# Kernel optimization log

Measured on AMD Instinct MI355X. Metric: run time of the kernel, lower is better.

Reference implementation:

```python
import jax, jax.numpy as jnp
import numpy as np

B, L, H = 256, 128, 512  # batch, max_len, hidden (en_hidden_size == de_hidden_size)


def setup_inputs() -> dict:
    key = jax.random.key(0)
    ks = jax.random.split(key, 12)
    xs = jax.random.randint(ks[0], (B, L), 0, 1000, dtype=jnp.int32)
    argsort_xs = jnp.argsort(xs, axis=1).astype(jnp.int32)  # teacher-forcing pointer targets
    x_lens = jnp.full((B,), L, dtype=jnp.int32)  # passed through but unused by the math
    s = 0.05
    p = lambda k, shp: jax.random.normal(k, shp, jnp.float32) * s
    return {
        "xs": xs, "x_lens": x_lens, "argsort_xs": argsort_xs,
        # encoder LSTM(1 -> H), PyTorch gate order i,f,g,o; b = b_ih + b_hh fused
        "enc_Wi": p(ks[1], (4 * H, 1)), "enc_Wh": p(ks[2], (4 * H, H)), "enc_b": p(ks[3], (4 * H,)),
        # decoder LSTM(H+1 -> H)
        "dec_Wi": p(ks[4], (4 * H, H + 1)), "dec_Wh": p(ks[5], (4 * H, H)), "dec_b": p(ks[6], (4 * H,)),
        # PtrNetAttention: w1, w2 [H,H] (bias-free Linear stores [out,in]), vt [1,H]
        "w1": p(ks[7], (H, H)), "w2": p(ks[8], (H, H)), "vt": p(ks[9], (1, H)),
    }


def _lstm_step(x, h, c, Wi, Wh, b):
    z = x @ Wi.T + h @ Wh.T + b
    i, f, g, o = jnp.split(z, 4, axis=-1)
    c = jax.nn.sigmoid(f) * c + jax.nn.sigmoid(i) * jnp.tanh(g)
    h = jax.nn.sigmoid(o) * jnp.tanh(c)
    return h, c


def _forward(xs, argsort_xs, enc_Wi, enc_Wh, enc_b, dec_Wi, dec_Wh, dec_b, w1, w2, vt):
    xf = xs.astype(jnp.float32)
    h0 = jnp.zeros((B, H), jnp.float32)
    c0 = jnp.zeros((B, H), jnp.float32)

    def enc_step(carry, x_t):
        h, c = carry
        h, c = _lstm_step(x_t[:, None], h, c, enc_Wi, enc_Wh, enc_b)
        return (h, c), h

    (h, c), enc_out = jax.lax.scan(enc_step, (h0, c0), xf.T)  # enc_out: [L,B,H]
    enc_out = enc_out.transpose(1, 0, 2)  # [B,L,H]
    enc_w1 = enc_out @ w1.T  # hoisted: w1(encoder_output), identical math each step

    def dec_step(carry, tf_idx):
        h, c, dec_in = carry
        # attention uses pre-update decoder hidden h (decoder_hidden[0][0])
        scores = jnp.tanh(enc_w1 + (h @ w2.T)[:, None, :]) @ vt[0]  # [B,L]
        aj = jax.nn.softmax(scores, axis=1)
        context = jnp.einsum('bl,blh->bh', aj, enc_out)
        x_in = jnp.concatenate([context, dec_in[:, None]], axis=-1)  # [B,H+1]
        h, c = _lstm_step(x_in, h, c, dec_Wi, dec_Wh, dec_b)
        # teacher-forced pointer: next input is xs[t, argsort_xs[t, i]]
        next_in = jnp.take_along_axis(xf, tf_idx[:, None], axis=1)[:, 0]
        return (h, c, next_in), jax.nn.log_softmax(scores, axis=1)

    dec_in0 = jnp.zeros((B,), jnp.float32)
    _, outs = jax.lax.scan(dec_step, (h, c, dec_in0), argsort_xs.T)  # [L,B,L]
    return outs.transpose(1, 0, 2)  # [B,L,L], matching decoder_outputs.permute(1,0,2)


def reference(xs, x_lens, argsort_xs, enc_Wi, enc_Wh, enc_b, dec_Wi, dec_Wh, dec_b, w1, w2, vt):
    return _forward(xs, argsort_xs, enc_Wi, enc_Wh, enc_b, dec_Wi, dec_Wh, dec_b, w1, w2, vt)
```

## Files before the change

### kernel.cpp

```cpp
#include <hip/hip_runtime.h>

#define BB 256
#define LL 128
#define HH 512
#define H4 2048

typedef unsigned short us;
typedef unsigned long long u64;
typedef __attribute__((ext_vector_type(8))) __bf16 bf16x8;
typedef __attribute__((ext_vector_type(4))) float f32x4;
typedef __attribute__((ext_vector_type(4))) int i32x4;

__device__ __forceinline__ float bf2f(us s) {
    unsigned u = ((unsigned)s) << 16;
    return __builtin_bit_cast(float, u);
}
__device__ __forceinline__ us f2bf(float f) {
    unsigned u = __builtin_bit_cast(unsigned, f);
    return (us)((u + 0x7fffu + ((u >> 16) & 1u)) >> 16);
}
__device__ __forceinline__ float sigm(float x) { return 1.f / (1.f + __expf(-x)); }
__device__ __forceinline__ float tanh_(float x) { return 1.f - 2.f / (1.f + __expf(2.f * x)); }
__device__ __forceinline__ bf16x8 ldb8(const us* p) { return *(const bf16x8*)(const void*)p; }

__device__ __forceinline__ bf16x8 ldb8_dev(const us* p) {
    union { u64 q[2]; bf16x8 v; } u;
    u.q[0] = __hip_atomic_load((const u64*)(const void*)p, __ATOMIC_RELAXED, __HIP_MEMORY_SCOPE_AGENT);
    u.q[1] = __hip_atomic_load((const u64*)(const void*)p + 1, __ATOMIC_RELAXED, __HIP_MEMORY_SCOPE_AGENT);
    return u.v;
}
__device__ __forceinline__ void st_pair_dev(us* p, unsigned myv, int lane) {
    unsigned ov = __shfl_xor(myv, 1);
    if (!(lane & 1)) {
        unsigned pk = (myv & 0xffffu) | (ov << 16);
        __hip_atomic_store((unsigned*)(void*)p, pk, __ATOMIC_RELAXED, __HIP_MEMORY_SCOPE_AGENT);
    }
}

__device__ __forceinline__ void gsync_nf(unsigned* flags, int myidx, int base, int n, unsigned target) {
    __syncthreads();
    if (threadIdx.x < 64) {
        if (threadIdx.x == 0)
            __hip_atomic_store(flags + (size_t)myidx * 16, target, __ATOMIC_RELAXED,
                               __HIP_MEMORY_SCOPE_AGENT);
        for (int i = (int)threadIdx.x; i < n; i += 64)
            while (__hip_atomic_load(flags + (size_t)(base + i) * 16, __ATOMIC_RELAXED,
                                     __HIP_MEMORY_SCOPE_AGENT) < target) {}
        asm volatile("" ::: "memory");
    }
    __syncthreads();
}

__device__ __forceinline__ void gsync_f(unsigned* flags, int myidx, int base, int n, unsigned target) {
    __syncthreads();
    if (threadIdx.x < 64) {
        if (threadIdx.x == 0) {
            __builtin_amdgcn_fence(__ATOMIC_RELEASE, "agent");
            __hip_atomic_store(flags + (size_t)myidx * 16, target, __ATOMIC_RELAXED,
                               __HIP_MEMORY_SCOPE_AGENT);
        }
        for (int i = (int)threadIdx.x; i < n; i += 64)
            while (__hip_atomic_load(flags + (size_t)(base + i) * 16, __ATOMIC_RELAXED,
                                     __HIP_MEMORY_SCOPE_AGENT) < target) {}
        __builtin_amdgcn_fence(__ATOMIC_ACQUIRE, "agent");
    }
    __syncthreads();
}

__device__ __forceinline__ bf16x8 ldfragA(const char* bufA, int l15, int quad, int kk) {
    int off = ((kk << 6) + (quad << 4)) ^ ((l15 & 7) << 4);
    return *(const bf16x8*)(bufA + (l15 << 10) + off);
}

extern "C" __global__ void __launch_bounds__(512) k_mega(
    const int* __restrict__ xs, const int* __restrict__ argsort,
    const float* __restrict__ enc_Wi, const float* __restrict__ enc_Wh, const float* __restrict__ enc_b,
    const float* __restrict__ dec_Wi, const float* __restrict__ dec_Wh, const float* __restrict__ dec_b,
    const float* __restrict__ w1, const float* __restrict__ w2, const float* __restrict__ vt,
    float* __restrict__ out, char* __restrict__ ws) {
    unsigned* flags = (unsigned*)ws;
    float* din = (float*)(ws + 524288);
    us* hdec = (us*)(ws + 526336);
    us* q = (us*)(ws + 1050624);
    us* ctx = (us*)(ws + 1312768);
    us* wiR = (us*)(ws + 1574912);
    float* wi_last = (float*)(ws + 3672064);
    us* whE = (us*)(ws + 3680256);
    us* whD = (us*)(ws + 5777408);
    us* w1B = (us*)(ws + 7874560);
    us* w2B = (us*)(ws + 8398848);
    us* enc_out = (us*)(ws + 8923136);
    us* enc_w1 = (us*)(ws + 42477568);

    extern __shared__ char smem[];
    us* eos = (us*)smem;
    char* bufA = smem + 131072;
    float* bufB = (float*)(smem + 147456);
    __shared__ float scs[LL];
    __shared__ float aj[LL];
    __shared__ float redm[2];
    __shared__ float reds[2];

    const int tid = threadIdx.x;
    const int lane = tid & 63;
    const int w = tid >> 6;
    const int l15 = lane & 15, quad = lane >> 4;
    const int blk = blockIdx.x;
    const int g = blk & 15;
    const int m = blk >> 4;
    const int b0 = g << 4;
    const int myflag = g * 16 + m;
    const int ct = w & 1;
    const int gate = w >> 1;
    const int c0 = ((m << 1) | ct) << 4;
    unsigned tgt = 0;

    auto stage_contig = [&](const us* src) {
        for (int e = tid; e < 1024; e += 512) {
            int row = e >> 6, bo = (e & 63) << 4;
            bf16x8 v = ldb8_dev(src + (e << 3));
            *(bf16x8*)(bufA + (row << 10) + (bo ^ ((row & 7) << 4))) = v;
        }
    };

    {
        int gt = blk * 512 + tid;
        for (int i = gt; i < H4 * HH; i += 131072) whE[i] = f2bf(enc_Wh[i]);
        for (int i = gt; i < H4 * HH; i += 131072) whD[i] = f2bf(dec_Wh[i]);
        for (int i = gt; i < HH * HH; i += 131072) w1B[i] = f2bf(w1[i]);
        for (int i = gt; i < HH * HH; i += 131072) w2B[i] = f2bf(w2[i]);
        for (int i = gt; i < H4 * HH; i += 131072)
            wiR[i] = f2bf(dec_Wi[(size_t)(i >> 9) * 513 + (i & 511)]);
        if (gt < H4) wi_last[gt] = dec_Wi[(size_t)gt * 513 + 512];
    }
    gsync_f(flags, myflag, 0, 256, ++tgt);

    float creg[4] = {0.f, 0.f, 0.f, 0.f};

    {
        bf16x8 whEf[16];
        {
            const us* Be = whE + (size_t)(gate * HH + c0 + l15) * HH + quad * 8;
#pragma unroll
            for (int kk = 0; kk < 16; ++kk) whEf[kk] = ldb8(Be + kk * 32);
        }
        float biE[4], wiE[4];
        if (w < 2) {
#pragma unroll
            for (int gg = 0; gg < 4; ++gg) {
                int rg = gg * HH + c0 + l15;
                biE[gg] = enc_b[rg];
                wiE[gg] = enc_Wi[rg];
            }
        }
        for (int t = 0; t < LL; ++t) {
            if (t > 0) {
                for (int e = tid; e < 1024; e += 512) {
                    int row = e >> 6, bo = (e & 63) << 4;
                    bf16x8 v = ldb8_dev(enc_out + ((size_t)(b0 + row) * LL + (t - 1)) * HH + (bo >> 1));
                    *(bf16x8*)(bufA + (row << 10) + (bo ^ ((row & 7) << 4))) = v;
                }
                __syncthreads();
                f32x4 acc = {};
#pragma unroll
                for (int kk = 0; kk < 16; ++kk)
                    acc = __builtin_amdgcn_mfma_f32_16x16x32_bf16(ldfragA(bufA, l15, quad, kk),
                                                                  whEf[kk], acc, 0, 0, 0);
#pragma unroll
                for (int r = 0; r < 4; ++r)
                    bufB[(ct * 4 + gate) * 256 + (quad * 4 + r) * 16 + l15] = acc[r];
                __syncthreads();
            }
            if (w < 2) {
#pragma unroll
                for (int r = 0; r < 4; ++r) {
                    int b = b0 + quad * 4 + r;
                    float xv = (float)xs[b * LL + t];
                    float zz[4];
#pragma unroll
                    for (int gg = 0; gg < 4; ++gg)
                        zz[gg] = (t > 0 ? bufB[(w * 4 + gg) * 256 + (quad * 4 + r) * 16 + l15] : 0.f)
                                 + biE[gg] + xv * wiE[gg];
                    float c_ = sigm(zz[1]) * creg[r] + sigm(zz[0]) * tanh_(zz[2]);
                    creg[r] = c_;
                    unsigned hv = (unsigned)f2bf(sigm(zz[3]) * tanh_(c_));
                    st_pair_dev(&enc_out[((size_t)b * LL + t) * HH + c0 + l15], hv, lane);
                    if (t == LL - 1) st_pair_dev(&hdec[(size_t)b * HH + c0 + l15], hv, lane);
                }
            }
            gsync_nf(flags, myflag, g * 16, 16, ++tgt);
        }
    }

    {
        int lw = m * 8 + w;
        for (int it = 0; it < 8; ++it) {
            int task = it * 128 + lw;
            int mt = task >> 3;
            int n0 = (task & 7) << 6;
            size_t m0 = (size_t)b0 * LL + (size_t)mt * 16;
            f32x4 acc[4] = {};
            const us* Ar = enc_out + (m0 + l15) * HH + quad * 8;
            const us* Br = w1B + (size_t)(n0 + l15) * HH + quad * 8;
#pragma unroll 8
            for (int kk = 0; kk < 16; ++kk) {
                bf16x8 a = ldb8(Ar + kk * 32);
#pragma unroll
                for (int tt = 0; tt < 4; ++tt) {
                    bf16x8 bv = ldb8(Br + (size_t)tt * 16 * HH + kk * 32);
                    acc[tt] = __builtin_amdgcn_mfma_f32_16x16x32_bf16(a, bv, acc[tt], 0, 0, 0);
                }
            }
#pragma unroll
            for (int tt = 0; tt < 4; ++tt)
#pragma unroll
                for (int r = 0; r < 4; ++r)
                    enc_w1[(m0 + quad * 4 + r) * HH + n0 + tt * 16 + l15] = f2bf(acc[tt][r]);
        }
    }
    gsync_f(flags, myflag, g * 16, 16, ++tgt);

    {
        const i32x4* src = (const i32x4*)(const void*)(enc_out + (size_t)(b0 + m) * LL * HH);
        i32x4* dst = (i32x4*)(void*)eos;
        for (int i = tid; i < 8192; i += 512) dst[i] = src[i];
    }
    bf16x8 ew1f[16];
    {
        const us* p = enc_w1 + ((size_t)(b0 + m) * LL + w) * HH + lane * 8;
#pragma unroll
        for (int i = 0; i < 16; ++i) ew1f[i] = ldb8(p + (size_t)i * 8 * HH);
    }
    __syncthreads();

    bf16x8 wiRf[16], whDf[16], w2f[4];
    {
        const us* Bw = wiR + (size_t)(gate * HH + c0 + l15) * HH + quad * 8;
        const us* Bh = whD + (size_t)(gate * HH + c0 + l15) * HH + quad * 8;
#pragma unroll
        for (int kk = 0; kk < 16; ++kk) {
            wiRf[kk] = ldb8(Bw + kk * 32);
            whDf[kk] = ldb8(Bh + kk * 32);
        }
        const us* Bq = w2B + (size_t)(c0 + l15) * HH + quad * 8;
#pragma unroll
        for (int j = 0; j < 4; ++j) w2f[j] = ldb8(Bq + (gate * 4 + j) * 32);
    }
    float biD[4], wlD[4];
    if (w < 2) {
#pragma unroll
        for (int gg = 0; gg < 4; ++gg) {
            int rg = gg * HH + c0 + l15;
            biD[gg] = dec_b[rg];
            wlD[gg] = wi_last[rg];
        }
    }

    for (int t = 0; t < LL; ++t) {
        const us* hcur = hdec + (size_t)(t & 1) * BB * HH;

        stage_contig(hcur + (size_t)b0 * HH);
        __syncthreads();
        {
            f32x4 acc = {};
#pragma unroll
            for (int j = 0; j < 4; ++j)
                acc = __builtin_amdgcn_mfma_f32_16x16x32_bf16(
                    ldfragA(bufA, l15, quad, gate * 4 + j), w2f[j], acc, 0, 0, 0);
#pragma unroll
            for (int r = 0; r < 4; ++r)
                bufB[(gate * 2 + ct) * 256 + (quad * 4 + r) * 16 + l15] = acc[r];
        }
        __syncthreads();
        if (w < 2) {
#pragma unroll
            for (int r = 0; r < 4; ++r) {
                float s = 0.f;
#pragma unroll
                for (int kq = 0; kq < 4; ++kq)
                    s += bufB[(kq * 2 + w) * 256 + (quad * 4 + r) * 16 + l15];
                st_pair_dev(&q[(size_t)(b0 + quad * 4 + r) * HH + c0 + l15],
                            (unsigned)f2bf(s), lane);
            }
        }
        gsync_nf(flags, myflag, g * 16, 16, ++tgt);

        {
            int b = b0 + m;
            int k0 = lane * 8;
            bf16x8 qv = ldb8_dev(q + (size_t)b * HH + k0);
            float qk[8], vtk[8];
#pragma unroll
            for (int j = 0; j < 8; ++j) {
                qk[j] = (float)qv[j];
                vtk[j] = vt[k0 + j];
            }
#pragma unroll 4
            for (int i = 0; i < 16; ++i) {
                int l = i * 8 + w;
                bf16x8 e8 = ew1f[i];
                float s = 0.f;
#pragma unroll
                for (int j = 0; j < 8; ++j) s += tanh_((float)e8[j] + qk[j]) * vtk[j];
#pragma unroll
                for (int off = 1; off < 64; off <<= 1) s += __shfl_xor(s, off);
                if (lane == 0) scs[l] = s;
            }
            __syncthreads();
            bool act = tid < 128;
            float sc = act ? scs[tid] : -1e30f;
            float mx = sc;
#pragma unroll
            for (int off = 1; off < 64; off <<= 1) mx = fmaxf(mx, __shfl_xor(mx, off));
            if (act && lane == 0) redm[w] = mx;
            __syncthreads();
            float M = fmaxf(redm[0], redm[1]);
            float e = act ? __expf(sc - M) : 0.f;
            float ss = e;
#pragma unroll
            for (int off = 1; off < 64; off <<= 1) ss += __shfl_xor(ss, off);
            if (act && lane == 0) reds[w] = ss;
            __syncthreads();
            float S = reds[0] + reds[1];
            if (act) {
                __builtin_nontemporal_store(sc - M - __logf(S), &out[((size_t)b * LL + t) * LL + tid]);
                aj[tid] = e / S;
            }
            __syncthreads();
            const us* ep = eos + tid;
            float cacc = 0.f;
#pragma unroll 16
            for (int l2 = 0; l2 < LL; ++l2) cacc += aj[l2] * bf2f(ep[(size_t)l2 * HH]);
            st_pair_dev(&ctx[(size_t)b * HH + tid], (unsigned)f2bf(cacc), tid & 63);
            if (tid == 0) {
                int idx = argsort[b * LL + t];
                __hip_atomic_store(&din[(size_t)((t + 1) & 1) * BB + b], (float)xs[b * LL + idx],
                                   __ATOMIC_RELAXED, __HIP_MEMORY_SCOPE_AGENT);
            }
        }
        gsync_nf(flags, myflag, g * 16, 16, ++tgt);

        {
            f32x4 zacc = {};
#pragma unroll
            for (int kk = 0; kk < 16; ++kk)
                zacc = __builtin_amdgcn_mfma_f32_16x16x32_bf16(ldfragA(bufA, l15, quad, kk),
                                                               whDf[kk], zacc, 0, 0, 0);
            __syncthreads();
            stage_contig(ctx + (size_t)b0 * HH);
            __syncthreads();
#pragma unroll
            for (int kk = 0; kk < 16; ++kk)
                zacc = __builtin_amdgcn_mfma_f32_16x16x32_bf16(ldfragA(bufA, l15, quad, kk),
                                                               wiRf[kk], zacc, 0, 0, 0);
#pragma unroll
            for (int r = 0; r < 4; ++r)
                bufB[(ct * 4 + gate) * 256 + (quad * 4 + r) * 16 + l15] = zacc[r];
        }
        __syncthreads();
        if (w < 2) {
            us* hnxt = hdec + (size_t)((t + 1) & 1) * BB * HH;
            const float* dcur = din + (size_t)(t & 1) * BB;
#pragma unroll
            for (int r = 0; r < 4; ++r) {
                int b = b0 + quad * 4 + r;
                float dv = (t == 0) ? 0.f
                                    : __hip_atomic_load((const float*)&dcur[b], __ATOMIC_RELAXED,
                                                        __HIP_MEMORY_SCOPE_AGENT);
                float zz[4];
#pragma unroll
                for (int gg = 0; gg < 4; ++gg)
                    zz[gg] = bufB[(w * 4 + gg) * 256 + (quad * 4 + r) * 16 + l15]
                             + biD[gg] + dv * wlD[gg];
                float c_ = sigm(zz[1]) * creg[r] + sigm(zz[0]) * tanh_(zz[2]);
                creg[r] = c_;
                st_pair_dev(&hnxt[(size_t)b * HH + c0 + l15],
                            (unsigned)f2bf(sigm(zz[3]) * tanh_(c_)), lane);
            }
        }
        gsync_nf(flags, myflag, g * 16, 16, ++tgt);
    }
}

extern "C" void kernel_launch(void* const* d_in, const int* in_sizes, int n_in,
                              void* d_out, int out_size, void* d_ws, size_t ws_size,
                              hipStream_t stream) {
    const int* xs = (const int*)d_in[0];
    const int* argsort = (const int*)d_in[2];
    const float* enc_Wi = (const float*)d_in[3];
    const float* enc_Wh = (const float*)d_in[4];
    const float* enc_b = (const float*)d_in[5];
    const float* dec_Wi = (const float*)d_in[6];
    const float* dec_Wh = (const float*)d_in[7];
    const float* dec_b = (const float*)d_in[8];
    const float* w1 = (const float*)d_in[9];
    const float* w2 = (const float*)d_in[10];
    const float* vt = (const float*)d_in[11];
    float* out = (float*)d_out;
    char* ws = (char*)d_ws;

    static bool attr_done = false;
    if (!attr_done) {
        hipFuncSetAttribute((const void*)k_mega, hipFuncAttributeMaxDynamicSharedMemorySize, 155648);
        attr_done = true;
    }

    hipMemsetAsync(ws, 0, 16384, stream);

    void* kargs[] = {&xs, &argsort, &enc_Wi, &enc_Wh, &enc_b, &dec_Wi, &dec_Wh, &dec_b,
                     &w1, &w2, &vt, &out, &ws};
    hipLaunchCooperativeKernel((void*)k_mega, dim3(256), dim3(512), kargs, 155648, stream);

    (void)in_sizes; (void)n_in; (void)out_size; (void)ws_size;
}
```

Baseline: 4.849 ms.

## Pack barrier flags contiguously, drop LDS enc_out staging, prefetch ctx into separate buffer

The grid-barrier flags are packed into contiguous words per group instead of one per 64-byte slot. Polling now uses 16 lanes with s_sleep backoff, which should cut cache-line traffic during the many per-step barriers. The 128KB LDS copy of enc_out is removed and the context reduction reads from global memory instead, so dynamic shared memory is no longer needed. Context rows are loaded into registers before the Wh MFMA and written to a second LDS buffer, which removes one __syncthreads; q is broadcast through LDS and vt is hoisted out of the loop. The trade-off is that context accumulation now reads global/L2 instead of LDS, and packed flags may cause false sharing on writes.

```diff
diff --git a/kernel.cpp b/kernel.cpp
--- a/kernel.cpp
+++ b/kernel.cpp
@@ -9,7 +9,6 @@
 typedef unsigned long long u64;
 typedef __attribute__((ext_vector_type(8))) __bf16 bf16x8;
 typedef __attribute__((ext_vector_type(4))) float f32x4;
-typedef __attribute__((ext_vector_type(4))) int i32x4;
 
 __device__ __forceinline__ float bf2f(us s) {
     unsigned u = ((unsigned)s) << 16;
@@ -37,39 +36,40 @@
     }
 }
 
-__device__ __forceinline__ void gsync_nf(unsigned* flags, int myidx, int base, int n, unsigned target) {
+__device__ __forceinline__ void gsync_nf(unsigned* flags, int g, int m, unsigned target) {
     __syncthreads();
-    if (threadIdx.x < 64) {
+    if (threadIdx.x < 16) {
         if (threadIdx.x == 0)
-            __hip_atomic_store(flags + (size_t)myidx * 16, target, __ATOMIC_RELAXED,
+            __hip_atomic_store(flags + g * 16 + m, target, __ATOMIC_RELAXED,
                                __HIP_MEMORY_SCOPE_AGENT);
-        for (int i = (int)threadIdx.x; i < n; i += 64)
-            while (__hip_atomic_load(flags + (size_t)(base + i) * 16, __ATOMIC_RELAXED,
-                                     __HIP_MEMORY_SCOPE_AGENT) < target) {}
+        while (__hip_atomic_load(flags + g * 16 + (int)threadIdx.x, __ATOMIC_RELAXED,
+                                 __HIP_MEMORY_SCOPE_AGENT) < target)
+            __builtin_amdgcn_s_sleep(1);
         asm volatile("" ::: "memory");
     }
     __syncthreads();
 }
 
-__device__ __forceinline__ void gsync_f(unsigned* flags, int myidx, int base, int n, unsigned target) {
+__device__ __forceinline__ void gsync_f(unsigned* flags, int g, int m, unsigned target) {
     __syncthreads();
     if (threadIdx.x < 64) {
         if (threadIdx.x == 0) {
             __builtin_amdgcn_fence(__ATOMIC_RELEASE, "agent");
-            __hip_atomic_store(flags + (size_t)myidx * 16, target, __ATOMIC_RELAXED,
+            __hip_atomic_store(flags + g * 16 + m, target, __ATOMIC_RELAXED,
                                __HIP_MEMORY_SCOPE_AGENT);
         }
-        for (int i = (int)threadIdx.x; i < n; i += 64)
-            while (__hip_atomic_load(flags + (size_t)(base + i) * 16, __ATOMIC_RELAXED,
-                                     __HIP_MEMORY_SCOPE_AGENT) < target) {}
+        for (int i = (int)threadIdx.x; i < 256; i += 64)
+            while (__hip_atomic_load(flags + i, __ATOMIC_RELAXED,
+                                     __HIP_MEMORY_SCOPE_AGENT) < target)
+                __builtin_amdgcn_s_sleep(1);
         __builtin_amdgcn_fence(__ATOMIC_ACQUIRE, "agent");
     }
     __syncthreads();
 }
 
-__device__ __forceinline__ bf16x8 ldfragA(const char* bufA, int l15, int quad, int kk) {
+__device__ __forceinline__ bf16x8 ldfragA(const char* buf, int l15, int quad, int kk) {
     int off = ((kk << 6) + (quad << 4)) ^ ((l15 & 7) << 4);
-    return *(const bf16x8*)(bufA + (l15 << 10) + off);
+    return *(const bf16x8*)(buf + (l15 << 10) + off);
 }
 
 extern "C" __global__ void __launch_bounds__(512) k_mega(
@@ -92,10 +92,10 @@
     us* enc_out = (us*)(ws + 8923136);
     us* enc_w1 = (us*)(ws + 42477568);
 
-    extern __shared__ char smem[];
-    us* eos = (us*)smem;
-    char* bufA = smem + 131072;
-    float* bufB = (float*)(smem + 147456);
+    __shared__ char bufA[16384];
+    __shared__ char bufC[16384];
+    __shared__ float bufB[2048];
+    __shared__ us qbuf[HH];
     __shared__ float scs[LL];
     __shared__ float aj[LL];
     __shared__ float redm[2];
@@ -109,7 +109,6 @@
     const int g = blk & 15;
     const int m = blk >> 4;
     const int b0 = g << 4;
-    const int myflag = g * 16 + m;
     const int ct = w & 1;
     const int gate = w >> 1;
     const int c0 = ((m << 1) | ct) << 4;
@@ -133,7 +132,7 @@
             wiR[i] = f2bf(dec_Wi[(size_t)(i >> 9) * 513 + (i & 511)]);
         if (gt < H4) wi_last[gt] = dec_Wi[(size_t)gt * 513 + 512];
     }
-    gsync_f(flags, myflag, 0, 256, ++tgt);
+    gsync_f(flags, g, m, ++tgt);
 
     float creg[4] = {0.f, 0.f, 0.f, 0.f};
 
@@ -188,7 +187,7 @@
                     if (t == LL - 1) st_pair_dev(&hdec[(size_t)b * HH + c0 + l15], hv, lane);
                 }
             }
-            gsync_nf(flags, myflag, g * 16, 16, ++tgt);
+            gsync_nf(flags, g, m, ++tgt);
         }
     }
 
@@ -218,20 +217,14 @@
                     enc_w1[(m0 + quad * 4 + r) * HH + n0 + tt * 16 + l15] = f2bf(acc[tt][r]);
         }
     }
-    gsync_f(flags, myflag, g * 16, 16, ++tgt);
-
-    {
-        const i32x4* src = (const i32x4*)(const void*)(enc_out + (size_t)(b0 + m) * LL * HH);
-        i32x4* dst = (i32x4*)(void*)eos;
-        for (int i = tid; i < 8192; i += 512) dst[i] = src[i];
-    }
+    gsync_f(flags, g, m, ++tgt);
+
     bf16x8 ew1f[16];
     {
         const us* p = enc_w1 + ((size_t)(b0 + m) * LL + w) * HH + lane * 8;
 #pragma unroll
         for (int i = 0; i < 16; ++i) ew1f[i] = ldb8(p + (size_t)i * 8 * HH);
     }
-    __syncthreads();
 
     bf16x8 wiRf[16], whDf[16], w2f[4];
     {
@@ -255,6 +248,9 @@
             wlD[gg] = wi_last[rg];
         }
     }
+    float vtk[8];
+#pragma unroll
+    for (int j = 0; j < 8; ++j) vtk[j] = vt[lane * 8 + j];
 
     for (int t = 0; t < LL; ++t) {
         const us* hcur = hdec + (size_t)(t & 1) * BB * HH;
@@ -283,18 +279,17 @@
                             (unsigned)f2bf(s), lane);
             }
         }
-        gsync_nf(flags, myflag, g * 16, 16, ++tgt);
+        gsync_nf(flags, g, m, ++tgt);
 
         {
             int b = b0 + m;
-            int k0 = lane * 8;
-            bf16x8 qv = ldb8_dev(q + (size_t)b * HH + k0);
-            float qk[8], vtk[8];
-#pragma unroll
-            for (int j = 0; j < 8; ++j) {
-                qk[j] = (float)qv[j];
-                vtk[j] = vt[k0 + j];
-            }
+            if (tid < 64)
+                *(bf16x8*)(void*)(qbuf + (tid << 3)) = ldb8_dev(q + (size_t)b * HH + (tid << 3));
+            __syncthreads();
+            bf16x8 qv = ldb8(qbuf + (lane << 3));
+            float qk[8];
+#pragma unroll
+            for (int j = 0; j < 8; ++j) qk[j] = (float)qv[j];
 #pragma unroll 4
             for (int i = 0; i < 16; ++i) {
                 int l = i * 8 + w;
@@ -327,9 +322,9 @@
                 aj[tid] = e / S;
             }
             __syncthreads();
-            const us* ep = eos + tid;
+            const us* ep = enc_out + (size_t)b * LL * HH + tid;
             float cacc = 0.f;
-#pragma unroll 16
+#pragma unroll 8
             for (int l2 = 0; l2 < LL; ++l2) cacc += aj[l2] * bf2f(ep[(size_t)l2 * HH]);
             st_pair_dev(&ctx[(size_t)b * HH + tid], (unsigned)f2bf(cacc), tid & 63);
             if (tid == 0) {
@@ -338,20 +333,26 @@
                                    __ATOMIC_RELAXED, __HIP_MEMORY_SCOPE_AGENT);
             }
         }
-        gsync_nf(flags, myflag, g * 16, 16, ++tgt);
+        gsync_nf(flags, g, m, ++tgt);
 
         {
+            bf16x8 cv0 = ldb8_dev(ctx + (size_t)b0 * HH + (tid << 3));
+            bf16x8 cv1 = ldb8_dev(ctx + (size_t)b0 * HH + ((tid + 512) << 3));
             f32x4 zacc = {};
 #pragma unroll
             for (int kk = 0; kk < 16; ++kk)
                 zacc = __builtin_amdgcn_mfma_f32_16x16x32_bf16(ldfragA(bufA, l15, quad, kk),
                                                                whDf[kk], zacc, 0, 0, 0);
-            __syncthreads();
-            stage_contig(ctx + (size_t)b0 * HH);
+            {
+                int e = tid, row = e >> 6, bo = (e & 63) << 4;
+                *(bf16x8*)(bufC + (row << 10) + (bo ^ ((row & 7) << 4))) = cv0;
+                e = tid + 512; row = e >> 6; bo = (e & 63) << 4;
+                *(bf16x8*)(bufC + (row << 10) + (bo ^ ((row & 7) << 4))) = cv1;
+            }
             __syncthreads();
 #pragma unroll
             for (int kk = 0; kk < 16; ++kk)
-                zacc = __builtin_amdgcn_mfma_f32_16x16x32_bf16(ldfragA(bufA, l15, quad, kk),
+                zacc = __builtin_amdgcn_mfma_f32_16x16x32_bf16(ldfragA(bufC, l15, quad, kk),
                                                                wiRf[kk], zacc, 0, 0, 0);
 #pragma unroll
             for (int r = 0; r < 4; ++r)
@@ -378,7 +379,7 @@
                             (unsigned)f2bf(sigm(zz[3]) * tanh_(c_)), lane);
             }
         }
-        gsync_nf(flags, myflag, g * 16, 16, ++tgt);
+        gsync_nf(flags, g, m, ++tgt);
     }
 }
 
@@ -399,17 +400,11 @@
     float* out = (float*)d_out;
     char* ws = (char*)d_ws;
 
-    static bool attr_done = false;
-    if (!attr_done) {
-        hipFuncSetAttribute((const void*)k_mega, hipFuncAttributeMaxDynamicSharedMemorySize, 155648);
-        attr_done = true;
-    }
-
-    hipMemsetAsync(ws, 0, 16384, stream);
+    hipMemsetAsync(ws, 0, 1024, stream);
 
     void* kargs[] = {&xs, &argsort, &enc_Wi, &enc_Wh, &enc_b, &dec_Wi, &dec_Wh, &dec_b,
                      &w1, &w2, &vt, &out, &ws};
-    hipLaunchCooperativeKernel((void*)k_mega, dim3(256), dim3(512), kargs, 155648, stream);
+    hipLaunchCooperativeKernel((void*)k_mega, dim3(256), dim3(512), kargs, 0, stream);
 
     (void)in_sizes; (void)n_in; (void)out_size; (void)ws_size;
 }
```

Result: slower. 8.466 ms (+74.6%).
